# Performance work log

Hardware: AMD Instinct MI355X
Metric: run time of the kernel (lower is better)

## Reference

```python
import jax, jax.numpy as jnp
import numpy as np

H = 256          # encoder hidden per direction
D = 2 * H        # decoder hidden / bidirectional feature dim
IN = 2
OUT = 2
B = 64
T = 256
STEPS = 24       # hard-coded decoder loop length in the source


def gru_cell(x, h, Wih, Whh, bih, bhh):
    # PyTorch GRU cell: gate order (r, z, n)
    gi = x @ Wih.T + bih
    gh = h @ Whh.T + bhh
    ir, iz, inn = jnp.split(gi, 3, axis=-1)
    hr, hz, hn = jnp.split(gh, 3, axis=-1)
    r = jax.nn.sigmoid(ir + hr)
    z = jax.nn.sigmoid(iz + hz)
    n = jnp.tanh(inn + r * hn)
    return (1.0 - z) * n + z * h


def run_dir(xs, Wih, Whh, bih, bhh, reverse):
    # xs: (T, B, F) time-major; returns outputs (T, B, H) and last hidden (B, H)
    h0 = jnp.zeros((xs.shape[1], Whh.shape[-1]), xs.dtype)
    def step(h, xt):
        h2 = gru_cell(xt, h, Wih, Whh, bih, bhh)
        return h2, h2
    h_last, ys = jax.lax.scan(step, h0, xs, reverse=reverse)
    return ys, h_last


def setup_inputs():
    keys = jax.random.split(jax.random.key(0), 24)
    k = iter(keys)
    def rn(shape, s):
        return jax.random.normal(next(k), shape, jnp.float32) * s
    se = 1.0 / np.sqrt(H)
    sd = 1.0 / np.sqrt(D)
    return {
        "x": rn((B, T, IN), 1.0),
        "enc_Wih0": rn((2, 3 * H, IN), se),
        "enc_Whh0": rn((2, 3 * H, H), se),
        "enc_bih0": rn((2, 3 * H), se),
        "enc_bhh0": rn((2, 3 * H), se),
        "enc_Wih": rn((2, 2, 3 * H, D), se),
        "enc_Whh": rn((2, 2, 3 * H, H), se),
        "enc_bih": rn((2, 2, 3 * H), se),
        "enc_bhh": rn((2, 2, 3 * H), se),
        "dec_Wih": rn((3, 3 * D, D), sd),
        "dec_Whh": rn((3, 3 * D, D), sd),
        "dec_bih": rn((3, 3 * D), sd),
        "dec_bhh": rn((3, 3 * D), sd),
        "fc_con_W": rn((D, 2 * D), sd),
        "fc_con_b": rn((D,), sd),
        "attn_W": rn((D, 2 * D), sd),
        "attn_b": rn((D,), sd),
        "v": jax.random.uniform(next(k), (D,), jnp.float32),  # torch.rand init
        "fc_W": rn((OUT, D), sd),
        "fc_b": rn((OUT,), sd),
    }


def reference(x, enc_Wih0, enc_Whh0, enc_bih0, enc_bhh0,
              enc_Wih, enc_Whh, enc_bih, enc_bhh,
              dec_Wih, dec_Whh, dec_bih, dec_bhh,
              fc_con_W, fc_con_b, attn_W, attn_b, v, fc_W, fc_b):
    # ---- bidirectional 3-layer GRU encoder ----
    seq = x.transpose(1, 0, 2)  # (T, B, IN) time-major
    hf_list, hb_list = [], []
    for l in range(3):
        if l == 0:
            Wf, Uf, bf, cf = enc_Wih0[0], enc_Whh0[0], enc_bih0[0], enc_bhh0[0]
            Wb, Ub, bb, cb = enc_Wih0[1], enc_Whh0[1], enc_bih0[1], enc_bhh0[1]
        else:
            Wf, Uf, bf, cf = enc_Wih[l-1, 0], enc_Whh[l-1, 0], enc_bih[l-1, 0], enc_bhh[l-1, 0]
            Wb, Ub, bb, cb = enc_Wih[l-1, 1], enc_Whh[l-1, 1], enc_bih[l-1, 1], enc_bhh[l-1, 1]
        yf, hf = run_dir(seq, Wf, Uf, bf, cf, False)
        yb, hb = run_dir(seq, Wb, Ub, bb, cb, True)
        seq = jnp.concatenate([yf, yb], axis=-1)
        hf_list.append(hf)
        hb_list.append(hb)
    enc_out = seq.transpose(1, 0, 2)  # (B, T, D)
    # hidden_decoder = cat(forward, backward) per layer -> (3, B, D)
    hidden = jnp.stack([jnp.concatenate([f, b], axis=-1)
                        for f, b in zip(hf_list, hb_list)])
    dec_in = enc_out[:, -1, :]  # (B, D)

    # additive attention: energy = tanh(W [h; enc_out] + b); precompute enc part
    attn_Wh = attn_W[:, :D]
    attn_We = attn_W[:, D:]
    enc_proj = jnp.einsum('bte,de->btd', enc_out, attn_We)  # (B, T, D)

    def dec_step(carry, _):
        d_in, hid = carry
        hq = hid[-1] @ attn_Wh.T                               # (B, D)
        energy = jnp.tanh(hq[:, None, :] + enc_proj + attn_b)  # (B, T, D)
        scores = jnp.einsum('btd,d->bt', energy, v)
        aw = jax.nn.softmax(scores, axis=1)                    # (B, T)
        ctx = jnp.einsum('bt,btd->bd', aw, enc_out)            # (B, D)
        inp = jnp.concatenate([d_in, ctx], axis=-1) @ fc_con_W.T + fc_con_b
        new_h = []
        for l in range(3):  # 3-layer unidirectional decoder GRU, single step
            hl = gru_cell(inp, hid[l], dec_Wih[l], dec_Whh[l], dec_bih[l], dec_bhh[l])
            new_h.append(hl)
            inp = hl
        out_step = inp @ fc_W.T + fc_b
        return (inp, jnp.stack(new_h)), out_step

    _, outs = jax.lax.scan(dec_step, (dec_in, hidden), None, length=STEPS)
    return outs.transpose(1, 0, 2)  # (B, 24, OUT)
```

## Files before the change

kernel.cpp:

```cpp
#include <hip/hip_runtime.h>

typedef unsigned short u16;
typedef unsigned int u32;
typedef _Float16 f16;
typedef f16   f16x2 __attribute__((ext_vector_type(2)));
typedef f16   f16x4 __attribute__((ext_vector_type(4)));
typedef f16   f16x8 __attribute__((ext_vector_type(8)));
typedef float f32x4 __attribute__((ext_vector_type(4)));

#define MFMA16(a,b,c) __builtin_amdgcn_mfma_f32_16x16x32_f16((a),(b),(c),0,0,0)

__device__ __forceinline__ float sigm_(float x){ return 1.f/(1.f + __expf(-x)); }
__device__ __forceinline__ float tanh_(float x){ return 1.f - 2.f/(1.f + __expf(2.f*x)); }
__device__ __forceinline__ float clampf(float x, float c){
  if (!(x > -c)) x = -c;
  if (x > c) x = c;
  return x;
}
__device__ __forceinline__ f16x8 cvt8f(const float* p){
  const float4 a = *(const float4*)p;
  const float4 b = *(const float4*)(p+4);
  f16x8 r;
  r[0]=(f16)a.x; r[1]=(f16)a.y; r[2]=(f16)a.z; r[3]=(f16)a.w;
  r[4]=(f16)b.x; r[5]=(f16)b.y; r[6]=(f16)b.z; r[7]=(f16)b.w;
  return r;
}

__device__ __forceinline__ void gbar_(u32* c, u32 nb){
  __syncthreads();
  __threadfence();
  if (threadIdx.x == 0) {
    __hip_atomic_fetch_add(c, 1u, __ATOMIC_RELAXED, __HIP_MEMORY_SCOPE_AGENT);
    while (__hip_atomic_load(c, __ATOMIC_RELAXED, __HIP_MEMORY_SCOPE_AGENT) < nb) {}
  }
  __syncthreads();
  __threadfence();
}

__global__ void k_diag(float* out, int mib){
  const int i = blockIdx.x*256 + threadIdx.x;
  if (i < 3072) out[i] = 1000.f * (float)mib;
}

__global__ void k_prep_dec(const float* dWhh, const float* attnW, const float* fccon,
                           const float* dWih, f16* R3)
{
  long idx = (long)blockIdx.x*256 + threadIdx.x;
  const float* src; int rs, colOff = 0, NKS; long dst, loc;
  if (idx < 294912L) {
    loc = idx; const int m = (int)(loc / 98304); loc %= 98304;
    src = dWhh + (long)m*786432; rs = 512; NKS = 16; dst = (long)m*786432;
  } else if (idx < 327680L) {
    loc = idx - 294912L; src = attnW; colOff = 512; rs = 1024; NKS = 16; dst = 2359296L;
  } else if (idx < 393216L) {
    loc = idx - 327680L; src = fccon; rs = 1024; NKS = 32; dst = 2621440L;
  } else if (idx < 688128L) {
    loc = idx - 393216L; const int m = (int)(loc / 98304); loc %= 98304;
    src = dWih + (long)m*786432; rs = 512; NKS = 16; dst = 3440640L + (long)m*786432;
  } else if (idx < 720896L) {
    loc = idx - 688128L; src = attnW; colOff = 0; rs = 1024; NKS = 16; dst = 5799936L;
  } else return;
  const int lane = (int)(loc & 63);
  const long frag = loc >> 6;
  const int ks = (int)(frag % NKS);
  const long nt = frag / NKS;
  const int n  = (int)(nt*16 + (lane & 15));
  const int k0 = ks*32 + ((lane >> 4) << 3);
  const float* sp = src + (long)n*rs + colOff + k0;
  f16* dp = R3 + dst + loc*8;
  #pragma unroll
  for (int j = 0; j < 8; ++j) dp[j] = (f16)sp[j];
}

__global__ void k_gi0s(const float* __restrict__ x, const float* __restrict__ W,
                       const float* __restrict__ bi, f16* __restrict__ gi,
                       int seg, int BH, int lbh, int b0)
{
  const long idx = (long)blockIdx.x*256 + threadIdx.x;
  const int v = (int)(idx % 24);
  long rest = idx / 24;
  const int tid = (int)(rest & 511); rest >>= 9;
  const int bq = (int)(rest & ((1 << (lbh-4)) - 1)); rest >>= (lbh-4);
  const int s = (int)(rest & 63);
  const int d = (int)(rest >> 6);
  const int r = v / 6, rem = v % 6, i = rem / 3, g = rem % 3;
  const int w = tid >> 6, q = (tid >> 4) & 3, lo = tid & 15;
  const int n = g*256 + (2*w + i)*16 + lo;
  const int b = bq*16 + q*4 + r;
  const int t = d ? (255 - (seg*64 + s)) : (seg*64 + s);
  const float x0 = x[(((b0+b)<<8) + t)*2];
  const float x1 = x[(((b0+b)<<8) + t)*2 + 1];
  const long wi = ((long)d*768 + n)*2;
  gi[idx] = (f16)clampf(x0*W[wi] + x1*W[wi+1] + bi[d*768 + n], 32.f);
}

#define GIE(G, vv) ((float)((vv) < 8 ? (G)[0][(vv)&7] : ((vv) < 16 ? (G)[1][(vv)-8] : (G)[2][(vv)-16])))

__global__ __launch_bounds__(512, 1) void k_enc_seg(
    const f16* __restrict__ gi, const float* __restrict__ Wraw,
    const float* __restrict__ bhh, f16* __restrict__ seq, int ostr,
    f16* __restrict__ fin, float* __restrict__ hcar, int seg, int BH)
{
  const int tid = threadIdx.x;
  const int w = tid >> 6, lane = tid & 63;
  const int lo16 = lane & 15, quad = lane >> 4;
  const int nbq = BH >> 4;
  const int dir = blockIdx.x / nbq, bq = blockIdx.x % nbq;

  __shared__ f16 h16[4][16][264];

  const float* mat = Wraw + (long)dir*196608;
  f16x8 wr[6][8];
  #pragma unroll
  for (int p = 0; p < 3; ++p)
    #pragma unroll
    for (int i = 0; i < 2; ++i) {
      const int n = (p*16 + 2*w + i)*16 + lo16;
      #pragma unroll
      for (int ks = 0; ks < 8; ++ks)
        wr[p*2+i][ks] = cvt8f(mat + (long)n*256 + ks*32 + quad*8);
    }
  float bh_[3][2];
  #pragma unroll
  for (int p = 0; p < 3; ++p)
    #pragma unroll
    for (int i = 0; i < 2; ++i)
      bh_[p][i] = bhh[dir*768 + p*256 + (2*w+i)*16 + lo16];

  float hreg[2][4];
  if (seg == 0) {
    #pragma unroll
    for (int i = 0; i < 2; ++i)
      #pragma unroll
      for (int r = 0; r < 4; ++r) {
        hreg[i][r] = 0.f;
        h16[0][quad*4 + r][(2*w+i)*16 + lo16] = (f16)0.f;
      }
  } else {
    #pragma unroll
    for (int i = 0; i < 2; ++i) {
      const int c = (2*w+i)*16 + lo16;
      #pragma unroll
      for (int r = 0; r < 4; ++r) {
        const float v = hcar[((dir*BH) + bq*16 + quad*4 + r)*256 + c];
        hreg[i][r] = v;
        h16[0][quad*4 + r][c] = (f16)v;
      }
    }
  }

  const long gstep = (long)nbq*512*24;
  const f16* gbase = gi + (((long)dir*64*nbq + bq)*512 + tid)*24;
  f16x8 g0[3], g1[3];
  { const f16x8* gp = (const f16x8*)gbase; g0[0]=gp[0]; g0[1]=gp[1]; g0[2]=gp[2]; }

  const int frow = tid >> 5;
  const int fcol = (tid & 31) * 8;

  for (int s = 0; s < 64; ++s) {
    __syncthreads();
    if (s >= 2) {
      const int so = s - 2;
      const int t2 = dir ? (255 - (seg*64 + so)) : (seg*64 + so);
      const f16x8 hv = *(const f16x8*)&h16[(so+1)&3][frow][fcol];
      *(f16x8*)&seq[((long)t2*ostr + bq*16 + frow)*512 + dir*256 + fcol] = hv;
    }
    f32x4 acc[6];
    #pragma unroll
    for (int q = 0; q < 6; ++q) acc[q] = (f32x4){0.f,0.f,0.f,0.f};
    #pragma unroll
    for (int ks = 0; ks < 8; ++ks) {
      const f16x8 a = *(const f16x8*)&h16[s&3][lo16][ks*32 + quad*8];
      #pragma unroll
      for (int q = 0; q < 6; ++q)
        acc[q] = MFMA16(a, wr[q][ks], acc[q]);
    }
    if (s < 63) {
      const f16x8* gp = (const f16x8*)(gbase + (long)(s+1)*gstep);
      g1[0]=gp[0]; g1[1]=gp[1]; g1[2]=gp[2];
    }
    #pragma unroll
    for (int i = 0; i < 2; ++i) {
      const int c = (2*w+i)*16 + lo16;
      #pragma unroll
      for (int r = 0; r < 4; ++r) {
        const int row = quad*4 + r;
        const int v = r*6 + i*3;
        const float gir = GIE(g0, v);
        const float giz = GIE(g0, v+1);
        const float gin = GIE(g0, v+2);
        const float rv = sigm_(gir + acc[i][r]   + bh_[0][i]);
        const float zv = sigm_(giz + acc[2+i][r] + bh_[1][i]);
        const float nv = tanh_(gin + rv*(acc[4+i][r] + bh_[2][i]));
        float hn = (1.f - zv)*nv + zv*hreg[i][r];
        hn = clampf(hn, 2.f);
        hreg[i][r] = hn;
        h16[(s+1)&3][row][c] = (f16)hn;
        if (seg == 3 && s == 63) fin[(bq*16 + row)*512 + dir*256 + c] = (f16)hn;
      }
    }
    g0[0]=g1[0]; g0[1]=g1[1]; g0[2]=g1[2];
  }
  __syncthreads();
  #pragma unroll
  for (int so = 62; so < 64; ++so) {
    const int t2 = dir ? (255 - (seg*64 + so)) : (seg*64 + so);
    const f16x8 hv = *(const f16x8*)&h16[(so+1)&3][frow][fcol];
    *(f16x8*)&seq[((long)t2*ostr + bq*16 + frow)*512 + dir*256 + fcol] = hv;
  }
  #pragma unroll
  for (int i = 0; i < 2; ++i) {
    const int c = (2*w+i)*16 + lo16;
    #pragma unroll
    for (int r = 0; r < 4; ++r)
      hcar[((dir*BH) + bq*16 + quad*4 + r)*256 + c] = hreg[i][r];
  }
}

__global__ void k_gemm_gi(const f16* __restrict__ A,
                          const float* __restrict__ Braw, long bzs,
                          const float* __restrict__ bias,
                          f16* __restrict__ gi,
                          int tb0, int tb1, int tdirsgn, int abstr, float cv)
{
  const int tid = threadIdx.x, w = tid>>6, lane = tid&63;
  const int lo16 = lane&15, quad = lane>>4;
  const int s_ = blockIdx.x;
  const int y  = blockIdx.y;
  const int z  = blockIdx.z;
  const int tbase = z ? tb1 : tb0;
  const int tdir  = z ? -tdirsgn : tdirsgn;
  const int mrow = s_*64 + w*16 + lo16;
  const long arow = (long)(tbase + tdir*(mrow >> 6))*abstr + (mrow & 63);
  const f16* Ap = A + arow*512 + quad*8;
  const float* Bp = Braw + (long)z*bzs;
  f32x4 acc[12];
  #pragma unroll
  for (int i=0;i<12;++i) acc[i]=(f32x4){0.f,0.f,0.f,0.f};
  for (int ks = 0; ks < 16; ++ks) {
    const f16x8 a = *(const f16x8*)(Ap + ks*32);
    #pragma unroll
    for (int g = 0; g < 3; ++g)
      #pragma unroll
      for (int jj = 0; jj < 4; ++jj) {
        const int n = g*256 + y*64 + jj*16 + lo16;
        const f16x8 b = cvt8f(Bp + (long)n*512 + ks*32 + quad*8);
        acc[g*4+jj] = MFMA16(a, b, acc[g*4+jj]);
      }
  }
  f16* base = gi + (((long)z*64 + s_)*4 + w)*12288L;
  #pragma unroll
  for (int l = 0; l < 2; ++l) {
    f16x8 rec8[3];
    #pragma unroll
    for (int r = 0; r < 4; ++r)
      #pragma unroll
      for (int jl = 0; jl < 2; ++jl)
        #pragma unroll
        for (int g = 0; g < 3; ++g) {
          const int nt = g*4 + l*2 + jl;
          const int n = g*256 + y*64 + (l*2+jl)*16 + lo16;
          const int slot = r*6 + jl*3 + g;
          rec8[slot>>3][slot&7] = (f16)clampf(acc[nt][r] + bias[z*768 + n], cv);
        }
    f16* dp = base + ((long)(y*2 + l)*64 + quad*16 + lo16)*24L;
    *(f16x8*)(dp)      = rec8[0];
    *(f16x8*)(dp + 8)  = rec8[1];
    *(f16x8*)(dp + 16) = rec8[2];
  }
}

__global__ void k_gemm(const f16* __restrict__ A, int K,
                       const f16* __restrict__ Bsw, const float* __restrict__ Braw,
                       long bzs, int ldb, int koff,
                       const float* __restrict__ bias, int biaszs,
                       void* __restrict__ Cv, long czs, int ldc, int mode,
                       int tb0, int tb1, int tdirsgn, int lbh, int abstr, float cv)
{
  const int tid = threadIdx.x, w = tid>>6, lane = tid&63;
  const int lo16 = lane&15, quad = lane>>4;
  const int m0 = blockIdx.x*64 + w*16;
  const int n0 = blockIdx.y*128;
  const int z  = blockIdx.z;
  const int tbase = z ? tb1 : tb0;
  const int tdir  = z ? -tdirsgn : tdirsgn;
  const int NKS = K >> 5;
  const int mrow = m0 + lo16;
  const long arow = (long)(tbase + tdir*(mrow >> lbh))*abstr + (mrow & ((1<<lbh)-1));
  const f16* Ap = A + arow*K + quad*8;
  f32x4 acc[8];
  #pragma unroll
  for (int i=0;i<8;++i) acc[i]=(f32x4){0.f,0.f,0.f,0.f};
  if (Bsw) {
    const f16* Bp = Bsw + (long)z*bzs;
    for (int ks = 0; ks < NKS; ++ks) {
      const f16x8 a = *(const f16x8*)(Ap + ks*32);
      #pragma unroll
      for (int nt = 0; nt < 8; ++nt) {
        const f16x8 b = *(const f16x8*)(Bp + (((long)((n0>>4)+nt)*NKS + ks) << 9) + lane*8);
        acc[nt] = MFMA16(a, b, acc[nt]);
      }
    }
  } else {
    const float* Bp = Braw + (long)z*bzs;
    for (int ks = 0; ks < NKS; ++ks) {
      const f16x8 a = *(const f16x8*)(Ap + ks*32);
      #pragma unroll
      for (int nt = 0; nt < 8; ++nt) {
        const f16x8 b = cvt8f(Bp + (long)(n0 + nt*16 + lo16)*ldb + koff + ks*32 + quad*8);
        acc[nt] = MFMA16(a, b, acc[nt]);
      }
    }
  }
  #pragma unroll
  for (int nt = 0; nt < 8; ++nt) {
    const int n = n0 + nt*16 + lo16;
    const float bv = bias ? bias[z*biaszs + n] : 0.f;
    #pragma unroll
    for (int r = 0; r < 4; ++r) {
      const int m = m0 + quad*4 + r;
      const float val = clampf(acc[nt][r] + bv, cv);
      if (mode == 2) {
        const int s_ = m >> lbh, b_ = m & ((1<<lbh)-1);
        const int bq_ = b_ >> 4, q_ = (b_ >> 2) & 3, r_ = b_ & 3;
        const int g_ = n >> 8, j_ = (n >> 4) & 15, lo_ = n & 15;
        const long idx = ((((long)z*64 + s_)*(1<<(lbh-4)) + bq_)*512
                          + ((j_>>1)*64 + q_*16 + lo_))*24 + r_*6 + (j_&1)*3 + g_;
        ((f16*)Cv)[idx] = (f16)val;
      } else if (mode == 3)
        ((f16*)Cv)[(((long)(m & 63) << 8) + (m >> 6))*512 + n] = (f16)val;
      else if (mode == 1)
        ((f16*)Cv)[(long)z*czs + (long)m*ldc + n] = (f16)val;
      else
        ((float*)Cv)[(long)z*czs + (long)m*ldc + n] = val;
    }
  }
}

__global__ void k_score(const f16* __restrict__ seq, const f16* __restrict__ We,
                        const float* __restrict__ hq, const float* __restrict__ ab,
                        const float* __restrict__ vp, float* __restrict__ S)
{
  const int t = blockIdx.x, tid = threadIdx.x;
  const int w = tid>>6, lane = tid&63, lo16 = lane&15, quad = lane>>4;
  __shared__ float svab[1024];
  for (int i = tid; i < 512; i += 256) { svab[i] = vp[i]; svab[512+i] = ab[i]; }
  __syncthreads();
  f32x4 acc[32];
  #pragma unroll
  for (int i=0;i<32;++i) acc[i]=(f32x4){0.f,0.f,0.f,0.f};
  const f16* Ap = seq + ((long)t*64 + w*16 + lo16)*512 + quad*8;
  for (int ks = 0; ks < 16; ++ks) {
    const f16x8 a = *(const f16x8*)(Ap + ks*32);
    #pragma unroll
    for (int nt = 0; nt < 32; ++nt) {
      const f16x8 b = *(const f16x8*)(We + (((long)nt*16 + ks) << 9) + lane*8);
      acc[nt] = MFMA16(a, b, acc[nt]);
    }
  }
  #pragma unroll
  for (int r = 0; r < 4; ++r) {
    const int b = w*16 + quad*4 + r;
    float sc = 0.f;
    #pragma unroll
    for (int nt = 0; nt < 32; ++nt) {
      const int n = nt*16 + lo16;
      sc += svab[n] * tanh_(acc[nt][r] + hq[(b<<9) + n] + svab[512+n]);
    }
    sc += __shfl_xor(sc, 1, 64); sc += __shfl_xor(sc, 2, 64);
    sc += __shfl_xor(sc, 4, 64); sc += __shfl_xor(sc, 8, 64);
    if (lo16 == 0) S[(b<<8) + t] = clampf(sc, 256.f);
  }
}

__global__ void k_attnctx(const float* __restrict__ S, const f16* __restrict__ enc,
                          f16* __restrict__ cat)
{
  const int b = blockIdx.x, tid = threadIdx.x;
  __shared__ float ssc[256], srd[256];
  const float sc = clampf(S[(b<<8) + tid], 256.f);
  srd[tid] = sc; __syncthreads();
  for (int off = 128; off > 0; off >>= 1) { if (tid < off) srd[tid] = fmaxf(srd[tid], srd[tid+off]); __syncthreads(); }
  const float mx = srd[0]; __syncthreads();
  const float e = __expf(sc - mx);
  srd[tid] = e; __syncthreads();
  for (int off = 128; off > 0; off >>= 1) { if (tid < off) srd[tid] += srd[tid+off]; __syncthreads(); }
  const float inv = 1.f / srd[0]; __syncthreads();
  ssc[tid] = e * inv; __syncthreads();
  float c0 = 0.f, c1 = 0.f;
  for (int tt = 0; tt < 256; ++tt) {
    const float awt = ssc[tt];
    const f16* ep = enc + (((long)tt*64 + b) << 9);
    c0 += awt * (float)ep[tid];
    c1 += awt * (float)ep[256 + tid];
  }
  cat[(b<<10) + 512 + tid] = (f16)clampf(c0, 4.f);
  cat[(b<<10) + 768 + tid] = (f16)clampf(c1, 4.f);
}

__global__ void k_dec_init(const f16* __restrict__ fin, const f16* __restrict__ seq,
                           f16* __restrict__ hb16, float* __restrict__ hf32,
                           f16* __restrict__ cat, u32* __restrict__ cnt)
{
  const int idx = blockIdx.x*256 + threadIdx.x;
  if (idx < 64) cnt[idx] = 0;
  const int d = idx & 511, b = (idx >> 9) & 63, l = idx >> 15;
  if (l < 3) {
    const float v = clampf((float)fin[((long)l<<15) + (b<<9) + d], 2.f);
    hb16[(long)l*65536 + (b<<9) + d] = (f16)v;
    hf32[(long)l*32768 + (b<<9) + d] = v;
  } else {
    cat[(b<<10) + d] = seq[((long)255*64 + b)*512 + d];
  }
}

__global__ __launch_bounds__(512, 1) void k_attn(
    const f16* __restrict__ seq, const f16* __restrict__ ep,
    const float* __restrict__ hf2, const f16* __restrict__ cat,
    const f16* __restrict__ whsw, const f16* __restrict__ fcsw,
    const float* __restrict__ fcconB, const float* __restrict__ vp,
    f16* __restrict__ inp, const float* __restrict__ fcW,
    const float* __restrict__ fcb, float* __restrict__ out, int step)
{
  const int b = blockIdx.x;
  const int tid = threadIdx.x, w = tid >> 6, lane = tid & 63;
  const int quad = lane >> 4;
  __shared__ float hsm[512];
  __shared__ float cats[1024];
  __shared__ float hqs[512];
  __shared__ float aw[256];
  __shared__ float red[8*512];
  hsm[tid]  = hf2[(b<<9) + tid];
  cats[tid] = (float)cat[(b<<10) + tid];
  __syncthreads();
  if (w < 2 && step > 0) {
    float p = 0.f;
    #pragma unroll
    for (int j = 0; j < 8; ++j) p += fcW[(w<<9) + lane*8 + j] * hsm[lane*8 + j];
    p += __shfl_xor(p,1,64); p += __shfl_xor(p,2,64); p += __shfl_xor(p,4,64);
    p += __shfl_xor(p,8,64); p += __shfl_xor(p,16,64); p += __shfl_xor(p,32,64);
    if (lane == 0) out[(b*24 + step-1)*2 + w] = clampf(p + fcb[w], 128.f);
  }
  #pragma unroll
  for (int i = 0; i < 4; ++i) {
    const int nt = w*4 + i;
    float p = 0.f;
    for (int ks = 0; ks < 16; ++ks) {
      const f16x8 wv = *(const f16x8*)(whsw + (((long)nt*16 + ks)<<9) + lane*8);
      const float4 ha = *(const float4*)&hsm[ks*32 + quad*8];
      const float4 hb = *(const float4*)&hsm[ks*32 + quad*8 + 4];
      p += (float)wv[0]*ha.x + (float)wv[1]*ha.y + (float)wv[2]*ha.z + (float)wv[3]*ha.w
         + (float)wv[4]*hb.x + (float)wv[5]*hb.y + (float)wv[6]*hb.z + (float)wv[7]*hb.w;
    }
    p += __shfl_xor(p,16,64); p += __shfl_xor(p,32,64);
    if (lane < 16) hqs[nt*16 + lane] = p;
  }
  __syncthreads();
  float hq8[8], v8[8];
  #pragma unroll
  for (int j = 0; j < 8; ++j) { hq8[j] = hqs[lane*8+j]; v8[j] = vp[lane*8+j]; }
  #pragma unroll 2
  for (int i = 0; i < 32; ++i) {
    const int t = w*32 + i;
    const f16x8 e = *(const f16x8*)(ep + (((long)(b<<8) + t)<<9) + lane*8);
    float s = 0.f;
    #pragma unroll
    for (int j = 0; j < 8; ++j) s += v8[j]*tanh_((float)e[j] + hq8[j]);
    s += __shfl_xor(s,1,64); s += __shfl_xor(s,2,64); s += __shfl_xor(s,4,64);
    s += __shfl_xor(s,8,64); s += __shfl_xor(s,16,64); s += __shfl_xor(s,32,64);
    if (lane == 0) aw[t] = clampf(s, 256.f);
  }
  __syncthreads();
  if (tid < 64) {
    float s0=aw[tid], s1=aw[tid+64], s2=aw[tid+128], s3=aw[tid+192];
    float mx = fmaxf(fmaxf(s0,s1), fmaxf(s2,s3));
    mx = fmaxf(mx, __shfl_xor(mx,1,64)); mx = fmaxf(mx, __shfl_xor(mx,2,64));
    mx = fmaxf(mx, __shfl_xor(mx,4,64)); mx = fmaxf(mx, __shfl_xor(mx,8,64));
    mx = fmaxf(mx, __shfl_xor(mx,16,64)); mx = fmaxf(mx, __shfl_xor(mx,32,64));
    const float e0=__expf(s0-mx), e1=__expf(s1-mx), e2=__expf(s2-mx), e3=__expf(s3-mx);
    float sm = e0+e1+e2+e3;
    sm += __shfl_xor(sm,1,64); sm += __shfl_xor(sm,2,64); sm += __shfl_xor(sm,4,64);
    sm += __shfl_xor(sm,8,64); sm += __shfl_xor(sm,16,64); sm += __shfl_xor(sm,32,64);
    const float inv = 1.f/sm;
    aw[tid]=e0*inv; aw[tid+64]=e1*inv; aw[tid+128]=e2*inv; aw[tid+192]=e3*inv;
  }
  __syncthreads();
  float c8[8];
  #pragma unroll
  for (int j = 0; j < 8; ++j) c8[j] = 0.f;
  #pragma unroll 2
  for (int i = 0; i < 32; ++i) {
    const int t = w*32 + i;
    const f16x8 e = *(const f16x8*)(seq + (((long)t*64 + b)<<9) + lane*8);
    const float awt = aw[t];
    #pragma unroll
    for (int j = 0; j < 8; ++j) c8[j] += awt*(float)e[j];
  }
  #pragma unroll
  for (int j = 0; j < 8; ++j) red[(w<<9) + lane*8 + j] = c8[j];
  __syncthreads();
  {
    float s = 0.f;
    #pragma unroll
    for (int ww = 0; ww < 8; ++ww) s += red[(ww<<9) + tid];
    cats[512 + tid] = clampf(s, 4.f);
  }
  __syncthreads();
  #pragma unroll
  for (int i = 0; i < 4; ++i) {
    const int nt = w*4 + i;
    float p = 0.f;
    for (int ks = 0; ks < 32; ++ks) {
      const f16x8 wv = *(const f16x8*)(fcsw + (((long)nt*32 + ks)<<9) + lane*8);
      const float4 ca = *(const float4*)&cats[ks*32 + quad*8];
      const float4 cb = *(const float4*)&cats[ks*32 + quad*8 + 4];
      p += (float)wv[0]*ca.x + (float)wv[1]*ca.y + (float)wv[2]*ca.z + (float)wv[3]*ca.w
         + (float)wv[4]*cb.x + (float)wv[5]*cb.y + (float)wv[6]*cb.z + (float)wv[7]*cb.w;
    }
    p += __shfl_xor(p,16,64); p += __shfl_xor(p,32,64);
    if (lane < 16) inp[(b<<9) + nt*16 + lane] = (f16)clampf(p + fcconB[nt*16+lane], 64.f);
  }
}

__global__ void k_cell3(const f16* __restrict__ inp0, const f16* __restrict__ WihSw,
                        const f16* __restrict__ WhhSw, const float* __restrict__ bihA,
                        const float* __restrict__ bhhA, float* __restrict__ hfA,
                        f16* __restrict__ hb, f16* __restrict__ cat, int p, u32* cnt)
{
  const int tid = threadIdx.x, w = tid>>6, lane = tid&63;
  const int lo16 = lane&15, quad = lane>>4;
  const int Wt = ((int)blockIdx.x & 7)*4 + w;
  const int mi = (int)blockIdx.x >> 3;
  for (int l = 0; l < 3; ++l) {
    const f16* inp = (l == 0) ? inp0 : (hb + (long)(2*(l-1) + (1-p))*32768);
    const f16* WihL = WihSw + (long)l*786432;
    const f16* WhhL = WhhSw + (long)l*786432;
    const float* bih = bihA + l*1536;
    const float* bhh = bhhA + l*1536;
    float* hf32 = hfA + (long)l*32768;
    const f16* hin = hb + (long)(2*l + p)*32768;
    f16* hout = hb + (long)(2*l + (1-p))*32768;
    f16* catp = (l == 2) ? cat : (f16*)nullptr;

    f32x4 arz[2], an_[2];
    #pragma unroll
    for (int i=0;i<2;++i){ arz[i]=(f32x4){0.f,0.f,0.f,0.f}; an_[i]=(f32x4){0.f,0.f,0.f,0.f}; }
    #pragma unroll 4
    for (int kk = 0; kk < 16; ++kk) {
      const f16x8 b0 = *(const f16x8*)(WihL + (((long)Wt*16 + kk)<<9)      + lane*8);
      const f16x8 b1 = *(const f16x8*)(WihL + (((long)(32+Wt)*16 + kk)<<9) + lane*8);
      const f16x8 b2 = *(const f16x8*)(WihL + (((long)(64+Wt)*16 + kk)<<9) + lane*8);
      const f16x8 a = *(const f16x8*)&inp[((mi*16 + lo16)<<9) + kk*32 + quad*8];
      arz[0] = MFMA16(a, b0, arz[0]);
      arz[1] = MFMA16(a, b1, arz[1]);
      an_[0] = MFMA16(a, b2, an_[0]);
    }
    #pragma unroll 4
    for (int kk = 0; kk < 16; ++kk) {
      const f16x8 b0 = *(const f16x8*)(WhhL + (((long)Wt*16 + kk)<<9)      + lane*8);
      const f16x8 b1 = *(const f16x8*)(WhhL + (((long)(32+Wt)*16 + kk)<<9) + lane*8);
      const f16x8 b2 = *(const f16x8*)(WhhL + (((long)(64+Wt)*16 + kk)<<9) + lane*8);
      const f16x8 a = *(const f16x8*)&hin[((mi*16 + lo16)<<9) + kk*32 + quad*8];
      arz[0] = MFMA16(a, b0, arz[0]);
      arz[1] = MFMA16(a, b1, arz[1]);
      an_[1] = MFMA16(a, b2, an_[1]);
    }
    const int c = Wt*16 + lo16;
    const float brz0 = bih[c]     + bhh[c];
    const float brz1 = bih[512+c] + bhh[512+c];
    const float bin_ = bih[1024+c];
    const float bhn_ = bhh[1024+c];
    #pragma unroll
    for (int r = 0; r < 4; ++r) {
      const int row = mi*16 + quad*4 + r;
      const float rv = sigm_(clampf(arz[0][r],64.f) + brz0);
      const float zv = sigm_(clampf(arz[1][r],64.f) + brz1);
      const float nv = tanh_(clampf(an_[0][r],64.f) + bin_ + rv*(clampf(an_[1][r],64.f) + bhn_));
      const float ho = hf32[(row<<9) + c];
      float hn2 = (1.f - zv)*nv + zv*ho;
      hn2 = clampf(hn2, 2.f);
      hf32[(row<<9) + c] = hn2;
      hout[(row<<9) + c] = (f16)hn2;
      if (catp) catp[(row<<10) + c] = (f16)hn2;
    }
    if (l < 2) gbar_(cnt + l, 32);
  }
}

__global__ void k_cell_raw(const f16* __restrict__ inp, const float* __restrict__ WihRaw,
                           const f16* __restrict__ WhhSw, const float* __restrict__ bih,
                           const float* __restrict__ bhh, float* __restrict__ hf32,
                           const f16* __restrict__ hin, f16* __restrict__ hout,
                           f16* __restrict__ cat)
{
  const int tid = threadIdx.x, w = tid>>6, lane = tid&63;
  const int lo16 = lane&15, quad = lane>>4;
  const int Wt = blockIdx.x*4 + w;
  f32x4 arz[8], an_[8];
  #pragma unroll
  for (int i=0;i<8;++i){ arz[i]=(f32x4){0.f,0.f,0.f,0.f}; an_[i]=(f32x4){0.f,0.f,0.f,0.f}; }
  const int nr = Wt*16 + lo16;
  const float* Rr = WihRaw + (long)nr*512        + quad*8;
  const float* Rz = WihRaw + (long)(512+nr)*512  + quad*8;
  const float* Rn = WihRaw + (long)(1024+nr)*512 + quad*8;
  #pragma unroll 2
  for (int kk = 0; kk < 16; ++kk) {
    const f16x8 b0 = cvt8f(Rr + kk*32);
    const f16x8 b1 = cvt8f(Rz + kk*32);
    const f16x8 b2 = cvt8f(Rn + kk*32);
    #pragma unroll
    for (int mi = 0; mi < 4; ++mi) {
      const f16x8 a = *(const f16x8*)&inp[((mi*16 + lo16)<<9) + kk*32 + quad*8];
      arz[mi]   = MFMA16(a, b0, arz[mi]);
      arz[4+mi] = MFMA16(a, b1, arz[4+mi]);
      an_[mi]   = MFMA16(a, b2, an_[mi]);
    }
  }
  #pragma unroll 2
  for (int kk = 0; kk < 16; ++kk) {
    const f16x8 b0 = *(const f16x8*)(WhhSw + (((long)Wt*16 + kk)<<9)      + lane*8);
    const f16x8 b1 = *(const f16x8*)(WhhSw + (((long)(32+Wt)*16 + kk)<<9) + lane*8);
    const f16x8 b2 = *(const f16x8*)(WhhSw + (((long)(64+Wt)*16 + kk)<<9) + lane*8);
    #pragma unroll
    for (int mi = 0; mi < 4; ++mi) {
      const f16x8 a = *(const f16x8*)&hin[((mi*16 + lo16)<<9) + kk*32 + quad*8];
      arz[mi]   = MFMA16(a, b0, arz[mi]);
      arz[4+mi] = MFMA16(a, b1, arz[4+mi]);
      an_[4+mi] = MFMA16(a, b2, an_[4+mi]);
    }
  }
  const int c = Wt*16 + lo16;
  const float brz0 = bih[c]     + bhh[c];
  const float brz1 = bih[512+c] + bhh[512+c];
  const float bin_ = bih[1024+c];
  const float bhn_ = bhh[1024+c];
  #pragma unroll
  for (int mi = 0; mi < 4; ++mi)
    #pragma unroll
    for (int r = 0; r < 4; ++r) {
      const int row = mi*16 + quad*4 + r;
      const float rv = sigm_(clampf(arz[mi][r],64.f)   + brz0);
      const float zv = sigm_(clampf(arz[4+mi][r],64.f) + brz1);
      const float nv = tanh_(clampf(an_[mi][r],64.f) + bin_ + rv*(clampf(an_[4+mi][r],64.f) + bhn_));
      const float ho = hf32[(row<<9) + c];
      float hn2 = (1.f - zv)*nv + zv*ho;
      hn2 = clampf(hn2, 2.f);
      hf32[(row<<9) + c] = hn2;
      hout[(row<<9) + c] = (f16)hn2;
      if (cat) cat[(row<<10) + c] = (f16)hn2;
    }
}

__global__ void k_out(const float* __restrict__ h2, const float* __restrict__ fcW,
                      const float* __restrict__ fcb, float* __restrict__ out, int step)
{
  const int b = blockIdx.x, t = threadIdx.x;
  __shared__ float r0[256], r1[256];
  const float ha = clampf(h2[(b<<9) + t], 2.f);
  const float hb = clampf(h2[(b<<9) + 256 + t], 2.f);
  r0[t] = ha*fcW[t]     + hb*fcW[256+t];
  r1[t] = ha*fcW[512+t] + hb*fcW[768+t];
  __syncthreads();
  for (int off = 128; off > 0; off >>= 1) {
    if (t < off) { r0[t] += r0[t+off]; r1[t] += r1[t+off]; }
    __syncthreads();
  }
  if (t == 0) {
    out[(b*24 + step)*2]     = clampf(r0[0] + fcb[0], 128.f);
    out[(b*24 + step)*2 + 1] = clampf(r1[0] + fcb[1], 128.f);
  }
}

extern "C" void kernel_launch(void* const* d_in, const int* in_sizes, int n_in,
                              void* d_out, int out_size, void* d_ws, size_t ws_size,
                              hipStream_t stream) {
  const float* X      = (const float*)d_in[0];
  const float* eWih0  = (const float*)d_in[1];
  const float* eWhh0  = (const float*)d_in[2];
  const float* ebih0  = (const float*)d_in[3];
  const float* ebhh0  = (const float*)d_in[4];
  const float* eWih   = (const float*)d_in[5];
  const float* eWhh   = (const float*)d_in[6];
  const float* ebih   = (const float*)d_in[7];
  const float* ebhh   = (const float*)d_in[8];
  const float* dWih   = (const float*)d_in[9];
  const float* dWhh   = (const float*)d_in[10];
  const float* dbih   = (const float*)d_in[11];
  const float* dbhh   = (const float*)d_in[12];
  const float* fcconW = (const float*)d_in[13];
  const float* fcconB = (const float*)d_in[14];
  const float* attnW  = (const float*)d_in[15];
  const float* attnB  = (const float*)d_in[16];
  const float* vW     = (const float*)d_in[17];
  const float* fcW    = (const float*)d_in[18];
  const float* fcB    = (const float*)d_in[19];
  float* OUT = (float*)d_out;

  const long need_big  = 47054848L;
  const long need_half = 32964608L;
  f16* H = (f16*)d_ws;
  f16 *SEQ = H, *L1OUT, *GIB, *R3, *FIN, *HB, *CAT, *INP;
  float *HC;
  int BH, lbh, nh, l1ostr, l1abstr; long gdir;

  if ((long)ws_size >= need_big) {
    BH = 64; lbh = 6; nh = 1; l1ostr = 64; l1abstr = 64;
    L1OUT = H + 8388608L;
    GIB   = H + 16777216L;
    HC    = (float*)(H + 23068672L);
    FIN   = H + 23134208L;
    HB    = H + 23232512L;
    CAT   = H + 23429120L;
    INP   = H + 23494656L;
    gdir  = 3145728L;
  } else if ((long)ws_size >= need_half) {
    BH = 32; lbh = 5; nh = 2; l1ostr = 32; l1abstr = 32;
    L1OUT = H + 8388608L;
    GIB   = H + 12582912L;
    HC    = (float*)(H + 16023552L);
    FIN   = H + 16089088L;
    HB    = H + 16187392L;
    CAT   = H + 16384000L;
    INP   = H + 16449536L;
    gdir  = 1572864L;
  } else {
    k_diag<<<12, 256, 0, stream>>>(OUT, (int)(ws_size >> 20));
    return;
  }
  R3 = GIB;
  float* ST = (float*)(GIB + 3145728L);
  float* HQ = ST;
  float* HF = ST + 32768;
  float* S  = ST + 131072;
  u32* CNT = (u32*)ST;
  const int nblk = 2*(BH>>4);
  const int gi0grid = (2*64*BH*768)/256;

  for (int h = 0; h < nh; ++h) {
    const int b0 = h*BH;
    for (int seg = 0; seg < 4; ++seg) {
      k_gi0s<<<gi0grid, 256, 0, stream>>>(X, eWih0, ebih0, GIB, seg, BH, lbh, b0);
      k_enc_seg<<<nblk, 512, 0, stream>>>(GIB, eWhh0, ebhh0, SEQ + (long)b0*512, 64,
                                          FIN + (long)b0*512, HC, seg, BH);
    }
    for (int seg = 0; seg < 4; ++seg) {
      if (BH == 64)
        k_gemm_gi<<<dim3(64, 4, 2), 256, 0, stream>>>(SEQ, eWih, 393216L, ebih,
            GIB, seg*64, 255 - seg*64, 1, 64, 32.f);
      else
        k_gemm<<<dim3(BH, 6, 2), 256, 0, stream>>>(SEQ + (long)b0*512, 512,
            (const f16*)nullptr, eWih, 393216L, 512, 0, ebih, 768,
            GIB, gdir, 768, 2, seg*64, 255 - seg*64, 1, lbh, 64, 32.f);
      k_enc_seg<<<nblk, 512, 0, stream>>>(GIB, eWhh, ebhh, L1OUT, l1ostr,
                                          FIN + 32768 + (long)b0*512, HC, seg, BH);
    }
    for (int seg = 0; seg < 4; ++seg) {
      if (BH == 64)
        k_gemm_gi<<<dim3(64, 4, 2), 256, 0, stream>>>(L1OUT, eWih + 2L*393216,
            393216L, ebih + 1536, GIB, seg*64, 255 - seg*64, 1, 64, 32.f);
      else
        k_gemm<<<dim3(BH, 6, 2), 256, 0, stream>>>(L1OUT, 512,
            (const f16*)nullptr, eWih + 2L*393216, 393216L, 512, 0, ebih + 1536, 768,
            GIB, gdir, 768, 2, seg*64, 255 - seg*64, 1, lbh, l1abstr, 32.f);
      k_enc_seg<<<nblk, 512, 0, stream>>>(GIB, eWhh + 2L*196608, ebhh + 1536,
                                          SEQ + (long)b0*512, 64,
                                          FIN + 65536 + (long)b0*512, HC, seg, BH);
    }
  }

  if (BH == 64) {
    f16* EP    = L1OUT;
    f16* WIHSW = GIB + 3440640L;
    f16* WHSW  = GIB + 5799936L;

    k_prep_dec<<<2816, 256, 0, stream>>>(dWhh, attnW, fcconW, dWih, R3);
    k_gemm<<<dim3(256, 4, 1), 256, 0, stream>>>(SEQ, 512,
        R3 + 2359296L, (const float*)nullptr, 0L, 0, 0, attnB, 0,
        EP, 0L, 512, 3, 0, 0, 1, 6, 64, 32.f);
    k_dec_init<<<512, 256, 0, stream>>>(FIN, SEQ, HB, HF, CAT, CNT);

    for (int s = 0; s < 24; ++s) {
      const int p = s & 1;
      k_attn<<<64, 512, 0, stream>>>(SEQ, EP, HF + 2*32768, CAT, WHSW, R3 + 2621440L,
          fcconB, vW, INP, fcW, fcB, OUT, s);
      k_cell3<<<32, 256, 0, stream>>>(INP, WIHSW, R3, dbih, dbhh, HF, HB, CAT,
          p, CNT + s*2);
    }
    k_out<<<64, 256, 0, stream>>>(HF + 2*32768, fcW, fcB, OUT, 23);
  } else {
    k_prep_dec<<<1536, 256, 0, stream>>>(dWhh, attnW, fcconW, dWih, R3);
    k_dec_init<<<512, 256, 0, stream>>>(FIN, SEQ, HB, HF, CAT, (u32*)(S + 16000));

    for (int s = 0; s < 24; ++s) {
      const int p = s & 1;
      const f16* h2in = HB + (4 + p)*32768L;
      k_gemm<<<dim3(1,4,1), 256, 0, stream>>>(h2in, 512,
          (const f16*)nullptr, attnW, 0L, 1024, 0, (const float*)nullptr, 0,
          HQ, 0L, 512, 0, 0, 0, 0, 6, 64, 64.f);
      k_score<<<256, 256, 0, stream>>>(SEQ, R3 + 2359296L, HQ, attnB, vW, S);
      k_attnctx<<<64, 256, 0, stream>>>(S, SEQ, CAT);
      k_gemm<<<dim3(1,4,1), 256, 0, stream>>>(CAT, 1024,
          R3 + 2621440L, (const float*)nullptr, 0L, 0, 0, fcconB, 0,
          INP, 0L, 512, 1, 0, 0, 0, 6, 64, 64.f);
      for (int l = 0; l < 3; ++l) {
        const f16* inp = (l == 0) ? INP : (HB + (2*(l-1) + (1-p))*32768L);
        k_cell_raw<<<8, 256, 0, stream>>>(inp,
                  dWih + (long)l*786432, R3 + (long)l*786432,
                  dbih + l*1536, dbhh + l*1536, HF + (long)l*32768,
                  HB + (2*l + p)*32768L, HB + (2*l + (1-p))*32768L,
                  (l == 2) ? CAT : (f16*)nullptr);
      }
      k_out<<<64, 256, 0, stream>>>(HF + 2*32768, fcW, fcB, OUT, s);
    }
  }
}
```

Measured before the change: 6.068 ms.

## Fuse decoder attention and GRU cells into one persistent kernel with grid barriers

Replaces the 48 per-step launches (attention kernel plus 3-layer cell kernel for each of 24 steps) with one persistent 64-block kernel. It loops over all decoder steps and uses global atomic barriers between the attention phase and each GRU layer. The aim is to remove kernel launch and drain overhead across the serial decoder loop. In exchange, the GRU phase now runs on only 2 of 8 waves per block, and each step adds grid barriers. Correctness relies on all 64 blocks being co-resident, and the counter-reset size grows to match.

```diff
diff --git a/kernel.cpp b/kernel.cpp
--- a/kernel.cpp
+++ b/kernel.cpp
@@ -403,7 +403,7 @@
                            f16* __restrict__ cat, u32* __restrict__ cnt)
 {
   const int idx = blockIdx.x*256 + threadIdx.x;
-  if (idx < 64) cnt[idx] = 0;
+  if (idx < 128) cnt[idx] = 0;
   const int d = idx & 511, b = (idx >> 9) & 63, l = idx >> 15;
   if (l < 3) {
     const float v = clampf((float)fin[((long)l<<15) + (b<<9) + d], 2.f);
@@ -414,176 +414,178 @@
   }
 }
 
-__global__ __launch_bounds__(512, 1) void k_attn(
+__global__ __launch_bounds__(512, 1) void k_dec_loop(
     const f16* __restrict__ seq, const f16* __restrict__ ep,
-    const float* __restrict__ hf2, const f16* __restrict__ cat,
+    f16* __restrict__ cat,
     const f16* __restrict__ whsw, const f16* __restrict__ fcsw,
     const float* __restrict__ fcconB, const float* __restrict__ vp,
     f16* __restrict__ inp, const float* __restrict__ fcW,
-    const float* __restrict__ fcb, float* __restrict__ out, int step)
+    const float* __restrict__ fcb, float* __restrict__ out,
+    const f16* __restrict__ WihSw, const f16* __restrict__ WhhSw,
+    const float* __restrict__ bihA, const float* __restrict__ bhhA,
+    float* __restrict__ hfA, f16* __restrict__ hb, u32* __restrict__ cnt)
 {
   const int b = blockIdx.x;
   const int tid = threadIdx.x, w = tid >> 6, lane = tid & 63;
-  const int quad = lane >> 4;
+  const int lo16 = lane & 15, quad = lane >> 4;
   __shared__ float hsm[512];
   __shared__ float cats[1024];
   __shared__ float hqs[512];
   __shared__ float aw[256];
   __shared__ float red[8*512];
-  hsm[tid]  = hf2[(b<<9) + tid];
-  cats[tid] = (float)cat[(b<<10) + tid];
-  __syncthreads();
-  if (w < 2 && step > 0) {
-    float p = 0.f;
-    #pragma unroll
-    for (int j = 0; j < 8; ++j) p += fcW[(w<<9) + lane*8 + j] * hsm[lane*8 + j];
-    p += __shfl_xor(p,1,64); p += __shfl_xor(p,2,64); p += __shfl_xor(p,4,64);
-    p += __shfl_xor(p,8,64); p += __shfl_xor(p,16,64); p += __shfl_xor(p,32,64);
-    if (lane == 0) out[(b*24 + step-1)*2 + w] = clampf(p + fcb[w], 128.f);
-  }
-  #pragma unroll
-  for (int i = 0; i < 4; ++i) {
-    const int nt = w*4 + i;
-    float p = 0.f;
-    for (int ks = 0; ks < 16; ++ks) {
-      const f16x8 wv = *(const f16x8*)(whsw + (((long)nt*16 + ks)<<9) + lane*8);
-      const float4 ha = *(const float4*)&hsm[ks*32 + quad*8];
-      const float4 hb = *(const float4*)&hsm[ks*32 + quad*8 + 4];
-      p += (float)wv[0]*ha.x + (float)wv[1]*ha.y + (float)wv[2]*ha.z + (float)wv[3]*ha.w
-         + (float)wv[4]*hb.x + (float)wv[5]*hb.y + (float)wv[6]*hb.z + (float)wv[7]*hb.w;
-    }
-    p += __shfl_xor(p,16,64); p += __shfl_xor(p,32,64);
-    if (lane < 16) hqs[nt*16 + lane] = p;
-  }
-  __syncthreads();
-  float hq8[8], v8[8];
-  #pragma unroll
-  for (int j = 0; j < 8; ++j) { hq8[j] = hqs[lane*8+j]; v8[j] = vp[lane*8+j]; }
-  #pragma unroll 2
-  for (int i = 0; i < 32; ++i) {
-    const int t = w*32 + i;
-    const f16x8 e = *(const f16x8*)(ep + (((long)(b<<8) + t)<<9) + lane*8);
-    float s = 0.f;
-    #pragma unroll
-    for (int j = 0; j < 8; ++j) s += v8[j]*tanh_((float)e[j] + hq8[j]);
-    s += __shfl_xor(s,1,64); s += __shfl_xor(s,2,64); s += __shfl_xor(s,4,64);
-    s += __shfl_xor(s,8,64); s += __shfl_xor(s,16,64); s += __shfl_xor(s,32,64);
-    if (lane == 0) aw[t] = clampf(s, 256.f);
-  }
-  __syncthreads();
-  if (tid < 64) {
-    float s0=aw[tid], s1=aw[tid+64], s2=aw[tid+128], s3=aw[tid+192];
-    float mx = fmaxf(fmaxf(s0,s1), fmaxf(s2,s3));
-    mx = fmaxf(mx, __shfl_xor(mx,1,64)); mx = fmaxf(mx, __shfl_xor(mx,2,64));
-    mx = fmaxf(mx, __shfl_xor(mx,4,64)); mx = fmaxf(mx, __shfl_xor(mx,8,64));
-    mx = fmaxf(mx, __shfl_xor(mx,16,64)); mx = fmaxf(mx, __shfl_xor(mx,32,64));
-    const float e0=__expf(s0-mx), e1=__expf(s1-mx), e2=__expf(s2-mx), e3=__expf(s3-mx);
-    float sm = e0+e1+e2+e3;
-    sm += __shfl_xor(sm,1,64); sm += __shfl_xor(sm,2,64); sm += __shfl_xor(sm,4,64);
-    sm += __shfl_xor(sm,8,64); sm += __shfl_xor(sm,16,64); sm += __shfl_xor(sm,32,64);
-    const float inv = 1.f/sm;
-    aw[tid]=e0*inv; aw[tid+64]=e1*inv; aw[tid+128]=e2*inv; aw[tid+192]=e3*inv;
-  }
-  __syncthreads();
-  float c8[8];
-  #pragma unroll
-  for (int j = 0; j < 8; ++j) c8[j] = 0.f;
-  #pragma unroll 2
-  for (int i = 0; i < 32; ++i) {
-    const int t = w*32 + i;
-    const f16x8 e = *(const f16x8*)(seq + (((long)t*64 + b)<<9) + lane*8);
-    const float awt = aw[t];
-    #pragma unroll
-    for (int j = 0; j < 8; ++j) c8[j] += awt*(float)e[j];
-  }
-  #pragma unroll
-  for (int j = 0; j < 8; ++j) red[(w<<9) + lane*8 + j] = c8[j];
-  __syncthreads();
-  {
-    float s = 0.f;
-    #pragma unroll
-    for (int ww = 0; ww < 8; ++ww) s += red[(ww<<9) + tid];
-    cats[512 + tid] = clampf(s, 4.f);
-  }
-  __syncthreads();
-  #pragma unroll
-  for (int i = 0; i < 4; ++i) {
-    const int nt = w*4 + i;
-    float p = 0.f;
-    for (int ks = 0; ks < 32; ++ks) {
-      const f16x8 wv = *(const f16x8*)(fcsw + (((long)nt*32 + ks)<<9) + lane*8);
-      const float4 ca = *(const float4*)&cats[ks*32 + quad*8];
-      const float4 cb = *(const float4*)&cats[ks*32 + quad*8 + 4];
-      p += (float)wv[0]*ca.x + (float)wv[1]*ca.y + (float)wv[2]*ca.z + (float)wv[3]*ca.w
-         + (float)wv[4]*cb.x + (float)wv[5]*cb.y + (float)wv[6]*cb.z + (float)wv[7]*cb.w;
-    }
-    p += __shfl_xor(p,16,64); p += __shfl_xor(p,32,64);
-    if (lane < 16) inp[(b<<9) + nt*16 + lane] = (f16)clampf(p + fcconB[nt*16+lane], 64.f);
-  }
-}
-
-__global__ void k_cell3(const f16* __restrict__ inp0, const f16* __restrict__ WihSw,
-                        const f16* __restrict__ WhhSw, const float* __restrict__ bihA,
-                        const float* __restrict__ bhhA, float* __restrict__ hfA,
-                        f16* __restrict__ hb, f16* __restrict__ cat, int p, u32* cnt)
-{
-  const int tid = threadIdx.x, w = tid>>6, lane = tid&63;
-  const int lo16 = lane&15, quad = lane>>4;
-  const int Wt = ((int)blockIdx.x & 7)*4 + w;
-  const int mi = (int)blockIdx.x >> 3;
-  for (int l = 0; l < 3; ++l) {
-    const f16* inp = (l == 0) ? inp0 : (hb + (long)(2*(l-1) + (1-p))*32768);
-    const f16* WihL = WihSw + (long)l*786432;
-    const f16* WhhL = WhhSw + (long)l*786432;
-    const float* bih = bihA + l*1536;
-    const float* bhh = bhhA + l*1536;
-    float* hf32 = hfA + (long)l*32768;
-    const f16* hin = hb + (long)(2*l + p)*32768;
-    f16* hout = hb + (long)(2*l + (1-p))*32768;
-    f16* catp = (l == 2) ? cat : (f16*)nullptr;
-
-    f32x4 arz[2], an_[2];
-    #pragma unroll
-    for (int i=0;i<2;++i){ arz[i]=(f32x4){0.f,0.f,0.f,0.f}; an_[i]=(f32x4){0.f,0.f,0.f,0.f}; }
-    #pragma unroll 4
-    for (int kk = 0; kk < 16; ++kk) {
-      const f16x8 b0 = *(const f16x8*)(WihL + (((long)Wt*16 + kk)<<9)      + lane*8);
-      const f16x8 b1 = *(const f16x8*)(WihL + (((long)(32+Wt)*16 + kk)<<9) + lane*8);
-      const f16x8 b2 = *(const f16x8*)(WihL + (((long)(64+Wt)*16 + kk)<<9) + lane*8);
-      const f16x8 a = *(const f16x8*)&inp[((mi*16 + lo16)<<9) + kk*32 + quad*8];
-      arz[0] = MFMA16(a, b0, arz[0]);
-      arz[1] = MFMA16(a, b1, arz[1]);
-      an_[0] = MFMA16(a, b2, an_[0]);
-    }
-    #pragma unroll 4
-    for (int kk = 0; kk < 16; ++kk) {
-      const f16x8 b0 = *(const f16x8*)(WhhL + (((long)Wt*16 + kk)<<9)      + lane*8);
-      const f16x8 b1 = *(const f16x8*)(WhhL + (((long)(32+Wt)*16 + kk)<<9) + lane*8);
-      const f16x8 b2 = *(const f16x8*)(WhhL + (((long)(64+Wt)*16 + kk)<<9) + lane*8);
-      const f16x8 a = *(const f16x8*)&hin[((mi*16 + lo16)<<9) + kk*32 + quad*8];
-      arz[0] = MFMA16(a, b0, arz[0]);
-      arz[1] = MFMA16(a, b1, arz[1]);
-      an_[1] = MFMA16(a, b2, an_[1]);
-    }
-    const int c = Wt*16 + lo16;
-    const float brz0 = bih[c]     + bhh[c];
-    const float brz1 = bih[512+c] + bhh[512+c];
-    const float bin_ = bih[1024+c];
-    const float bhn_ = bhh[1024+c];
-    #pragma unroll
-    for (int r = 0; r < 4; ++r) {
-      const int row = mi*16 + quad*4 + r;
-      const float rv = sigm_(clampf(arz[0][r],64.f) + brz0);
-      const float zv = sigm_(clampf(arz[1][r],64.f) + brz1);
-      const float nv = tanh_(clampf(an_[0][r],64.f) + bin_ + rv*(clampf(an_[1][r],64.f) + bhn_));
-      const float ho = hf32[(row<<9) + c];
-      float hn2 = (1.f - zv)*nv + zv*ho;
-      hn2 = clampf(hn2, 2.f);
-      hf32[(row<<9) + c] = hn2;
-      hout[(row<<9) + c] = (f16)hn2;
-      if (catp) catp[(row<<10) + c] = (f16)hn2;
-    }
-    if (l < 2) gbar_(cnt + l, 32);
+  const float* hf2 = hfA + 2*32768;
+
+  for (int s = 0; s < 24; ++s) {
+    const int p = s & 1;
+    hsm[tid]  = hf2[(b<<9) + tid];
+    cats[tid] = (float)cat[(b<<10) + tid];
+    __syncthreads();
+    if (w < 2 && s > 0) {
+      float pr = 0.f;
+      #pragma unroll
+      for (int j = 0; j < 8; ++j) pr += fcW[(w<<9) + lane*8 + j] * hsm[lane*8 + j];
+      pr += __shfl_xor(pr,1,64); pr += __shfl_xor(pr,2,64); pr += __shfl_xor(pr,4,64);
+      pr += __shfl_xor(pr,8,64); pr += __shfl_xor(pr,16,64); pr += __shfl_xor(pr,32,64);
+      if (lane == 0) out[(b*24 + s-1)*2 + w] = clampf(pr + fcb[w], 128.f);
+    }
+    #pragma unroll
+    for (int i = 0; i < 4; ++i) {
+      const int nt = w*4 + i;
+      float pr = 0.f;
+      for (int ks = 0; ks < 16; ++ks) {
+        const f16x8 wv = *(const f16x8*)(whsw + (((long)nt*16 + ks)<<9) + lane*8);
+        const float4 ha = *(const float4*)&hsm[ks*32 + quad*8];
+        const float4 hbv = *(const float4*)&hsm[ks*32 + quad*8 + 4];
+        pr += (float)wv[0]*ha.x + (float)wv[1]*ha.y + (float)wv[2]*ha.z + (float)wv[3]*ha.w
+            + (float)wv[4]*hbv.x + (float)wv[5]*hbv.y + (float)wv[6]*hbv.z + (float)wv[7]*hbv.w;
+      }
+      pr += __shfl_xor(pr,16,64); pr += __shfl_xor(pr,32,64);
+      if (lane < 16) hqs[nt*16 + lane] = pr;
+    }
+    __syncthreads();
+    float hq8[8], v8[8];
+    #pragma unroll
+    for (int j = 0; j < 8; ++j) { hq8[j] = hqs[lane*8+j]; v8[j] = vp[lane*8+j]; }
+    #pragma unroll 2
+    for (int i = 0; i < 32; ++i) {
+      const int t = w*32 + i;
+      const f16x8 e = *(const f16x8*)(ep + (((long)(b<<8) + t)<<9) + lane*8);
+      float sc = 0.f;
+      #pragma unroll
+      for (int j = 0; j < 8; ++j) sc += v8[j]*tanh_((float)e[j] + hq8[j]);
+      sc += __shfl_xor(sc,1,64); sc += __shfl_xor(sc,2,64); sc += __shfl_xor(sc,4,64);
+      sc += __shfl_xor(sc,8,64); sc += __shfl_xor(sc,16,64); sc += __shfl_xor(sc,32,64);
+      if (lane == 0) aw[t] = clampf(sc, 256.f);
+    }
+    __syncthreads();
+    if (tid < 64) {
+      float s0=aw[tid], s1=aw[tid+64], s2=aw[tid+128], s3=aw[tid+192];
+      float mx = fmaxf(fmaxf(s0,s1), fmaxf(s2,s3));
+      mx = fmaxf(mx, __shfl_xor(mx,1,64)); mx = fmaxf(mx, __shfl_xor(mx,2,64));
+      mx = fmaxf(mx, __shfl_xor(mx,4,64)); mx = fmaxf(mx, __shfl_xor(mx,8,64));
+      mx = fmaxf(mx, __shfl_xor(mx,16,64)); mx = fmaxf(mx, __shfl_xor(mx,32,64));
+      const float e0=__expf(s0-mx), e1=__expf(s1-mx), e2=__expf(s2-mx), e3=__expf(s3-mx);
+      float sm = e0+e1+e2+e3;
+      sm += __shfl_xor(sm,1,64); sm += __shfl_xor(sm,2,64); sm += __shfl_xor(sm,4,64);
+      sm += __shfl_xor(sm,8,64); sm += __shfl_xor(sm,16,64); sm += __shfl_xor(sm,32,64);
+      const float inv = 1.f/sm;
+      aw[tid]=e0*inv; aw[tid+64]=e1*inv; aw[tid+128]=e2*inv; aw[tid+192]=e3*inv;
+    }
+    __syncthreads();
+    float c8[8];
+    #pragma unroll
+    for (int j = 0; j < 8; ++j) c8[j] = 0.f;
+    #pragma unroll 2
+    for (int i = 0; i < 32; ++i) {
+      const int t = w*32 + i;
+      const f16x8 e = *(const f16x8*)(seq + (((long)t*64 + b)<<9) + lane*8);
+      const float awt = aw[t];
+      #pragma unroll
+      for (int j = 0; j < 8; ++j) c8[j] += awt*(float)e[j];
+    }
+    #pragma unroll
+    for (int j = 0; j < 8; ++j) red[(w<<9) + lane*8 + j] = c8[j];
+    __syncthreads();
+    {
+      float sm = 0.f;
+      #pragma unroll
+      for (int ww = 0; ww < 8; ++ww) sm += red[(ww<<9) + tid];
+      cats[512 + tid] = clampf(sm, 4.f);
+    }
+    __syncthreads();
+    #pragma unroll
+    for (int i = 0; i < 4; ++i) {
+      const int nt = w*4 + i;
+      float pr = 0.f;
+      for (int ks = 0; ks < 32; ++ks) {
+        const f16x8 wv = *(const f16x8*)(fcsw + (((long)nt*32 + ks)<<9) + lane*8);
+        const float4 ca = *(const float4*)&cats[ks*32 + quad*8];
+        const float4 cb = *(const float4*)&cats[ks*32 + quad*8 + 4];
+        pr += (float)wv[0]*ca.x + (float)wv[1]*ca.y + (float)wv[2]*ca.z + (float)wv[3]*ca.w
+            + (float)wv[4]*cb.x + (float)wv[5]*cb.y + (float)wv[6]*cb.z + (float)wv[7]*cb.w;
+      }
+      pr += __shfl_xor(pr,16,64); pr += __shfl_xor(pr,32,64);
+      if (lane < 16) inp[(b<<9) + nt*16 + lane] = (f16)clampf(pr + fcconB[nt*16+lane], 64.f);
+    }
+    gbar_(cnt + s*4, 64);
+    for (int l = 0; l < 3; ++l) {
+      if (w < 2) {
+        const int jid = (b<<1) + w;
+        const int Wt = jid & 31, mi = jid >> 5;
+        const f16* inl = (l == 0) ? inp : (hb + (long)(2*(l-1) + (1-p))*32768);
+        const f16* WihL = WihSw + (long)l*786432;
+        const f16* WhhL = WhhSw + (long)l*786432;
+        const float* bih = bihA + l*1536;
+        const float* bhh = bhhA + l*1536;
+        float* hf32 = hfA + (long)l*32768;
+        const f16* hin = hb + (long)(2*l + p)*32768;
+        f16* hout = hb + (long)(2*l + (1-p))*32768;
+        f16* catp = (l == 2) ? cat : (f16*)nullptr;
+
+        f32x4 arz[2], an_[2];
+        #pragma unroll
+        for (int i=0;i<2;++i){ arz[i]=(f32x4){0.f,0.f,0.f,0.f}; an_[i]=(f32x4){0.f,0.f,0.f,0.f}; }
+        #pragma unroll 4
+        for (int kk = 0; kk < 16; ++kk) {
+          const f16x8 b0 = *(const f16x8*)(WihL + (((long)Wt*16 + kk)<<9)      + lane*8);
+          const f16x8 b1 = *(const f16x8*)(WihL + (((long)(32+Wt)*16 + kk)<<9) + lane*8);
+          const f16x8 b2 = *(const f16x8*)(WihL + (((long)(64+Wt)*16 + kk)<<9) + lane*8);
+          const f16x8 a = *(const f16x8*)&inl[((mi*16 + lo16)<<9) + kk*32 + quad*8];
+          arz[0] = MFMA16(a, b0, arz[0]);
+          arz[1] = MFMA16(a, b1, arz[1]);
+          an_[0] = MFMA16(a, b2, an_[0]);
+        }
+        #pragma unroll 4
+        for (int kk = 0; kk < 16; ++kk) {
+          const f16x8 b0 = *(const f16x8*)(WhhL + (((long)Wt*16 + kk)<<9)      + lane*8);
+          const f16x8 b1 = *(const f16x8*)(WhhL + (((long)(32+Wt)*16 + kk)<<9) + lane*8);
+          const f16x8 b2 = *(const f16x8*)(WhhL + (((long)(64+Wt)*16 + kk)<<9) + lane*8);
+          const f16x8 a = *(const f16x8*)&hin[((mi*16 + lo16)<<9) + kk*32 + quad*8];
+          arz[0] = MFMA16(a, b0, arz[0]);
+          arz[1] = MFMA16(a, b1, arz[1]);
+          an_[1] = MFMA16(a, b2, an_[1]);
+        }
+        const int c = Wt*16 + lo16;
+        const float brz0 = bih[c]     + bhh[c];
+        const float brz1 = bih[512+c] + bhh[512+c];
+        const float bin_ = bih[1024+c];
+        const float bhn_ = bhh[1024+c];
+        #pragma unroll
+        for (int r = 0; r < 4; ++r) {
+          const int row = mi*16 + quad*4 + r;
+          const float rv = sigm_(clampf(arz[0][r],64.f) + brz0);
+          const float zv = sigm_(clampf(arz[1][r],64.f) + brz1);
+          const float nv = tanh_(clampf(an_[0][r],64.f) + bin_ + rv*(clampf(an_[1][r],64.f) + bhn_));
+          const float ho = hf32[(row<<9) + c];
+          float hn2 = (1.f - zv)*nv + zv*ho;
+          hn2 = clampf(hn2, 2.f);
+          hf32[(row<<9) + c] = hn2;
+          hout[(row<<9) + c] = (f16)hn2;
+          if (catp) catp[(row<<10) + c] = (f16)hn2;
+        }
+      }
+      gbar_(cnt + s*4 + 1 + l, 64);
+    }
   }
 }
 
@@ -779,13 +781,9 @@
         EP, 0L, 512, 3, 0, 0, 1, 6, 64, 32.f);
     k_dec_init<<<512, 256, 0, stream>>>(FIN, SEQ, HB, HF, CAT, CNT);
 
-    for (int s = 0; s < 24; ++s) {
-      const int p = s & 1;
-      k_attn<<<64, 512, 0, stream>>>(SEQ, EP, HF + 2*32768, CAT, WHSW, R3 + 2621440L,
-          fcconB, vW, INP, fcW, fcB, OUT, s);
-      k_cell3<<<32, 256, 0, stream>>>(INP, WIHSW, R3, dbih, dbhh, HF, HB, CAT,
-          p, CNT + s*2);
-    }
+    k_dec_loop<<<64, 512, 0, stream>>>(SEQ, EP, CAT, WHSW, R3 + 2621440L,
+        fcconB, vW, INP, fcW, fcB, OUT,
+        WIHSW, R3, dbih, dbhh, HF, HB, CNT);
     k_out<<<64, 256, 0, stream>>>(HF + 2*32768, fcW, fcB, OUT, 23);
   } else {
     k_prep_dec<<<1536, 256, 0, stream>>>(dWhh, attnW, fcconW, dWih, R3);
```

Measured after the change: 11.37 ms. +87.3%, slower.
